# Kernel optimization log

Measured on AMD Instinct MI355X. Metric: run time of the kernel, lower is better.

## Reference

```python
import jax, jax.numpy as jnp
import numpy as np

B, C, H, W = 16, 512, 64, 64


def setup_inputs() -> dict:
    key = jax.random.key(0)
    k1, k2 = jax.random.split(key)
    img_feat = jax.random.normal(k1, (B, C, H, W), dtype=jnp.float32)
    text_feat = jax.random.normal(k2, (B, C, H, W), dtype=jnp.float32)
    gamma = jnp.zeros((1,), dtype=jnp.float32)
    return {"img_feat": img_feat, "text_feat": text_feat, "gamma": gamma}


def reference(img_feat, text_feat, gamma):
    b, c, h, w = img_feat.shape
    q = img_feat.reshape(b, c, h * w)          # [B, C, HW]
    kv = text_feat.reshape(b, c, h * w)        # [B, C, HW]
    # channel-attention map: [B, C, C]
    attn = jnp.einsum('bcn,bdn->bcd', q, kv)
    attn = jax.nn.softmax(attn, axis=-1)
    info = jnp.einsum('bcd,bdn->bcn', attn, kv).reshape(b, c, h, w)
    return gamma * info + img_feat
```

## Files before the change

kernel.cpp:

```cpp
#include <hip/hip_runtime.h>
#include <hip/hip_bf16.h>


constexpr int NB = 16;
constexpr int NC = 512;
constexpr int NHW = 4096;
constexpr int SPLITK = 4;

typedef float f32x4 __attribute__((ext_vector_type(4)));
typedef __bf16 bf16x4 __attribute__((ext_vector_type(4)));
typedef __bf16 bf16x8 __attribute__((ext_vector_type(8)));

template <int STAGEF32, int EPI, int MDIM, int NDIM, int KDIM, int SPLITS>
__global__ __launch_bounds__(512) void gemm_bt(
    const void* __restrict__ Ap, const void* __restrict__ Bp,
    float* __restrict__ Dp, const float* __restrict__ img,
    const float* __restrict__ gammap, float* __restrict__ outp) {
  __shared__ __bf16 sA[128 * 64];
  __shared__ __bf16 sB[128 * 64];

  const int t = threadIdx.x;
  const int lane = t & 63;
  const int wave = t >> 6;
  const int wr = wave >> 2;
  const int wc = wave & 3;

  const int batch = blockIdx.z / SPLITS;
  const int split = blockIdx.z % SPLITS;

  const long aBatch = (long)batch * MDIM * KDIM;
  const long bBatch = (long)batch * NDIM * KDIM;
  const int aRow0 = blockIdx.x * 128;
  const int bRow0 = blockIdx.y * 128;

  constexpr int KSUB = KDIM / SPLITS;
  const int kBeg = split * KSUB;
  const int kEnd = kBeg + KSUB;

  f32x4 acc[4][2] = {};

  for (int k0 = kBeg; k0 < kEnd; k0 += 64) {
    if constexpr (STAGEF32) {
      const float* A = (const float*)Ap + aBatch;
      const float* Bm = (const float*)Bp + bBatch;
      const int c4 = (t & 15) * 4;
      const int rb = t >> 4;
#pragma unroll
      for (int i = 0; i < 4; ++i) {
        const int r = rb + 32 * i;
        f32x4 va = *(const f32x4*)(A + (long)(aRow0 + r) * KDIM + k0 + c4);
        f32x4 vb = *(const f32x4*)(Bm + (long)(bRow0 + r) * KDIM + k0 + c4);
        const int idx = r * 64 + (c4 ^ ((r & 7) << 3));
        bf16x4 ha = {(__bf16)va.x, (__bf16)va.y, (__bf16)va.z, (__bf16)va.w};
        bf16x4 hb = {(__bf16)vb.x, (__bf16)vb.y, (__bf16)vb.z, (__bf16)vb.w};
        *(bf16x4*)&sA[idx] = ha;
        *(bf16x4*)&sB[idx] = hb;
      }
    } else {
      const __bf16* A = (const __bf16*)Ap + aBatch;
      const __bf16* Bm = (const __bf16*)Bp + bBatch;
      const int c8 = (t & 7) * 8;
      const int rb = t >> 3;
#pragma unroll
      for (int i = 0; i < 2; ++i) {
        const int r = rb + 64 * i;
        bf16x8 va = *(const bf16x8*)(A + (long)(aRow0 + r) * KDIM + k0 + c8);
        bf16x8 vb = *(const bf16x8*)(Bm + (long)(bRow0 + r) * KDIM + k0 + c8);
        const int idx = r * 64 + (c8 ^ ((r & 7) << 3));
        *(bf16x8*)&sA[idx] = va;
        *(bf16x8*)&sB[idx] = vb;
      }
    }
    __syncthreads();

#pragma unroll
    for (int kk = 0; kk < 2; ++kk) {
      const int kb = kk * 32 + ((lane >> 4) << 3);
      bf16x8 af[4], bfr[2];
#pragma unroll
      for (int m = 0; m < 4; ++m) {
        const int r = wr * 64 + m * 16 + (lane & 15);
        af[m] = *(const bf16x8*)&sA[r * 64 + (kb ^ ((r & 7) << 3))];
      }
#pragma unroll
      for (int n = 0; n < 2; ++n) {
        const int r = wc * 32 + n * 16 + (lane & 15);
        bfr[n] = *(const bf16x8*)&sB[r * 64 + (kb ^ ((r & 7) << 3))];
      }
#pragma unroll
      for (int m = 0; m < 4; ++m)
#pragma unroll
        for (int n = 0; n < 2; ++n)
          acc[m][n] = __builtin_amdgcn_mfma_f32_16x16x32_bf16(
              af[m], bfr[n], acc[m][n], 0, 0, 0);
    }
    __syncthreads();
  }

  if constexpr (EPI == 0) {
    float* D = Dp + ((long)split * NB + batch) * MDIM * NDIM;
    const int m0 = aRow0 + wr * 64;
    const int n0 = bRow0 + wc * 32;
#pragma unroll
    for (int m = 0; m < 4; ++m)
#pragma unroll
      for (int n = 0; n < 2; ++n) {
        const int row0 = m0 + m * 16 + ((lane >> 4) << 2);
        const int col = n0 + n * 16 + (lane & 15);
#pragma unroll
        for (int r = 0; r < 4; ++r)
          D[(long)(row0 + r) * NDIM + col] = acc[m][n][r];
      }
  } else {
    const float g = gammap[0];
    const long obase = (long)batch * NC * NHW;
    const int sp0 = aRow0 + wr * 64;
    const int ch0 = bRow0 + wc * 32;
#pragma unroll
    for (int m = 0; m < 4; ++m)
#pragma unroll
      for (int n = 0; n < 2; ++n) {
        const int sp = sp0 + m * 16 + ((lane >> 4) << 2);
        const int ch = ch0 + n * 16 + (lane & 15);
        const long idx = obase + (long)ch * NHW + sp;
        f32x4 iv = *(const f32x4*)(img + idx);
        f32x4 ov;
#pragma unroll
        for (int r = 0; r < 4; ++r) ov[r] = g * acc[m][n][r] + iv[r];
        *(f32x4*)(outp + idx) = ov;
      }
  }
}

__global__ __launch_bounds__(256) void transpose_cast(
    const float* __restrict__ kv, __bf16* __restrict__ kvT) {
  __shared__ __bf16 tile[64 * 68];
  const int t = threadIdx.x;
  const int n0 = blockIdx.x * 64;
  const int d0 = blockIdx.y * 64;
  const long ibase = (long)blockIdx.z * NC * NHW;

  const int nc4 = (t & 15) * 4;
  const int dr0 = t >> 4;
#pragma unroll
  for (int i = 0; i < 4; ++i) {
    const int dr = dr0 + 16 * i;
    f32x4 v = *(const f32x4*)(kv + ibase + (long)(d0 + dr) * NHW + n0 + nc4);
    bf16x4 h = {(__bf16)v.x, (__bf16)v.y, (__bf16)v.z, (__bf16)v.w};
    *(bf16x4*)&tile[dr * 68 + nc4] = h;
  }
  __syncthreads();

  const long obase = (long)blockIdx.z * NHW * NC;
  const int nr = t >> 2;
  const int dc0 = t & 3;
#pragma unroll
  for (int i = 0; i < 2; ++i) {
    const int dc = dc0 + 4 * i;
    bf16x8 pk;
#pragma unroll
    for (int j = 0; j < 8; ++j) pk[j] = tile[(dc * 8 + j) * 68 + nr];
    *(bf16x8*)(kvT + obase + (long)(n0 + nr) * NC + d0 + dc * 8) = pk;
  }
}

__global__ __launch_bounds__(256) void softmax_rows(
    const float* __restrict__ attn, __bf16* __restrict__ P) {
  const int row = blockIdx.x * 4 + (threadIdx.x >> 6);
  const int lane = threadIdx.x & 63;
  const long PS = (long)NB * NC * NC;
  const float* src = attn + (long)row * NC;

  float x[8] = {0.f, 0.f, 0.f, 0.f, 0.f, 0.f, 0.f, 0.f};
#pragma unroll
  for (int s = 0; s < SPLITK; ++s) {
    f32x4 v0 = *(const f32x4*)(src + s * PS + lane * 4);
    f32x4 v1 = *(const f32x4*)(src + s * PS + 256 + lane * 4);
#pragma unroll
    for (int r = 0; r < 4; ++r) { x[r] += v0[r]; x[4 + r] += v1[r]; }
  }

  float mx = x[0];
#pragma unroll
  for (int r = 1; r < 8; ++r) mx = fmaxf(mx, x[r]);
#pragma unroll
  for (int off = 32; off >= 1; off >>= 1) mx = fmaxf(mx, __shfl_xor(mx, off));

  float e[8], s = 0.f;
#pragma unroll
  for (int r = 0; r < 8; ++r) { e[r] = expf(x[r] - mx); s += e[r]; }
#pragma unroll
  for (int off = 32; off >= 1; off >>= 1) s += __shfl_xor(s, off);
  const float inv = 1.0f / s;

  __bf16* dst = P + (long)row * NC;
  bf16x4 h0, h1;
#pragma unroll
  for (int r = 0; r < 4; ++r) {
    h0[r] = (__bf16)(e[r] * inv);
    h1[r] = (__bf16)(e[4 + r] * inv);
  }
  *(bf16x4*)(dst + lane * 4) = h0;
  *(bf16x4*)(dst + 256 + lane * 4) = h1;
}

extern "C" void kernel_launch(void* const* d_in, const int* in_sizes, int n_in,
                              void* d_out, int out_size, void* d_ws,
                              size_t ws_size, hipStream_t stream) {
  const float* img = (const float*)d_in[0];
  const float* txt = (const float*)d_in[1];
  const float* gamma = (const float*)d_in[2];
  float* out = (float*)d_out;

  char* ws = (char*)d_ws;
  float* attnP = (float*)ws;
  __bf16* kvT = (__bf16*)ws;
  __bf16* P = (__bf16*)(ws + (size_t)64 * 1024 * 1024);

  gemm_bt<1, 0, NC, NC, NHW, SPLITK>
      <<<dim3(NC / 128, NC / 128, NB * SPLITK), 512, 0, stream>>>(
          img, txt, attnP, nullptr, nullptr, nullptr);

  softmax_rows<<<dim3(NB * NC / 4), 256, 0, stream>>>(attnP, P);

  transpose_cast<<<dim3(NHW / 64, NC / 64, NB), 256, 0, stream>>>(txt, kvT);

  gemm_bt<0, 1, NHW, NC, NC, 1>
      <<<dim3(NHW / 128, NC / 128, NB), 512, 0, stream>>>(
          kvT, P, nullptr, img, gamma, out);
}
```

Measured before the change: 258.0 us.

## Prefetch next K tile into registers and remap workgroup order across XCDs

The GEMM main loop now issues global loads for the next K tile into registers before running the MFMA work on the current shared-memory tile, then writes them to LDS after a barrier. This hides global-memory latency behind compute at the cost of extra registers. Workgroup indices are also remapped so that consecutive blocks land in contiguous chunks across the 8 XCDs, which should improve L2 reuse of shared A/B rows.

```diff
diff --git a/kernel.cpp b/kernel.cpp
--- a/kernel.cpp
+++ b/kernel.cpp
@@ -25,13 +25,23 @@
   const int wr = wave >> 2;
   const int wc = wave & 3;
 
-  const int batch = blockIdx.z / SPLITS;
-  const int split = blockIdx.z % SPLITS;
+  constexpr int GX = MDIM / 128;
+  constexpr int GY = NDIM / 128;
+  constexpr int NWG = GX * GY * NB * SPLITS;
+  constexpr int QX = NWG / 8;
+  int flat = blockIdx.x + GX * (blockIdx.y + GY * blockIdx.z);
+  flat = (flat & 7) * QX + (flat >> 3);
+  const int bx = flat % GX;
+  const int by = (flat / GX) % GY;
+  const int bz = flat / (GX * GY);
+
+  const int batch = bz / SPLITS;
+  const int split = bz % SPLITS;
 
   const long aBatch = (long)batch * MDIM * KDIM;
   const long bBatch = (long)batch * NDIM * KDIM;
-  const int aRow0 = blockIdx.x * 128;
-  const int bRow0 = blockIdx.y * 128;
+  const int aRow0 = bx * 128;
+  const int bRow0 = by * 128;
 
   constexpr int KSUB = KDIM / SPLITS;
   const int kBeg = split * KSUB;
@@ -39,7 +49,10 @@
 
   f32x4 acc[4][2] = {};
 
-  for (int k0 = kBeg; k0 < kEnd; k0 += 64) {
+  f32x4 ra[4], rb4[4];
+  bf16x8 ha8[2], hb8[2];
+
+  auto stage_load = [&](int k0) {
     if constexpr (STAGEF32) {
       const float* A = (const float*)Ap + aBatch;
       const float* Bm = (const float*)Bp + bBatch;
@@ -48,13 +61,8 @@
 #pragma unroll
       for (int i = 0; i < 4; ++i) {
         const int r = rb + 32 * i;
-        f32x4 va = *(const f32x4*)(A + (long)(aRow0 + r) * KDIM + k0 + c4);
-        f32x4 vb = *(const f32x4*)(Bm + (long)(bRow0 + r) * KDIM + k0 + c4);
-        const int idx = r * 64 + (c4 ^ ((r & 7) << 3));
-        bf16x4 ha = {(__bf16)va.x, (__bf16)va.y, (__bf16)va.z, (__bf16)va.w};
-        bf16x4 hb = {(__bf16)vb.x, (__bf16)vb.y, (__bf16)vb.z, (__bf16)vb.w};
-        *(bf16x4*)&sA[idx] = ha;
-        *(bf16x4*)&sB[idx] = hb;
+        ra[i] = *(const f32x4*)(A + (long)(aRow0 + r) * KDIM + k0 + c4);
+        rb4[i] = *(const f32x4*)(Bm + (long)(bRow0 + r) * KDIM + k0 + c4);
       }
     } else {
       const __bf16* A = (const __bf16*)Ap + aBatch;
@@ -64,15 +72,41 @@
 #pragma unroll
       for (int i = 0; i < 2; ++i) {
         const int r = rb + 64 * i;
-        bf16x8 va = *(const bf16x8*)(A + (long)(aRow0 + r) * KDIM + k0 + c8);
-        bf16x8 vb = *(const bf16x8*)(Bm + (long)(bRow0 + r) * KDIM + k0 + c8);
+        ha8[i] = *(const bf16x8*)(A + (long)(aRow0 + r) * KDIM + k0 + c8);
+        hb8[i] = *(const bf16x8*)(Bm + (long)(bRow0 + r) * KDIM + k0 + c8);
+      }
+    }
+  };
+
+  auto stage_write = [&]() {
+    if constexpr (STAGEF32) {
+      const int c4 = (t & 15) * 4;
+      const int rb = t >> 4;
+#pragma unroll
+      for (int i = 0; i < 4; ++i) {
+        const int r = rb + 32 * i;
+        const int idx = r * 64 + (c4 ^ ((r & 7) << 3));
+        bf16x4 ha = {(__bf16)ra[i].x, (__bf16)ra[i].y, (__bf16)ra[i].z,
+                     (__bf16)ra[i].w};
+        bf16x4 hb = {(__bf16)rb4[i].x, (__bf16)rb4[i].y, (__bf16)rb4[i].z,
+                     (__bf16)rb4[i].w};
+        *(bf16x4*)&sA[idx] = ha;
+        *(bf16x4*)&sB[idx] = hb;
+      }
+    } else {
+      const int c8 = (t & 7) * 8;
+      const int rb = t >> 3;
+#pragma unroll
+      for (int i = 0; i < 2; ++i) {
+        const int r = rb + 64 * i;
         const int idx = r * 64 + (c8 ^ ((r & 7) << 3));
-        *(bf16x8*)&sA[idx] = va;
-        *(bf16x8*)&sB[idx] = vb;
-      }
-    }
-    __syncthreads();
-
+        *(bf16x8*)&sA[idx] = ha8[i];
+        *(bf16x8*)&sB[idx] = hb8[i];
+      }
+    }
+  };
+
+  auto compute_tile = [&]() {
 #pragma unroll
     for (int kk = 0; kk < 2; ++kk) {
       const int kb = kk * 32 + ((lane >> 4) << 3);
@@ -94,7 +128,22 @@
           acc[m][n] = __builtin_amdgcn_mfma_f32_16x16x32_bf16(
               af[m], bfr[n], acc[m][n], 0, 0, 0);
     }
+  };
+
+  stage_load(kBeg);
+  stage_write();
+  __syncthreads();
+
+#pragma unroll 1
+  for (int k0 = kBeg; k0 < kEnd; k0 += 64) {
+    const bool more = (k0 + 64) < kEnd;
+    if (more) stage_load(k0 + 64);
+    compute_tile();
     __syncthreads();
+    if (more) {
+      stage_write();
+      __syncthreads();
+    }
   }
 
   if constexpr (EPI == 0) {
```

Result: faster. 230.3 us (-10.7%).
